# Kernel tuning notes

Hardware: AMD Instinct MI355X
Metric: run time of the kernel (lower is better)

## Reference

```python
import jax, jax.numpy as jnp
import numpy as np


def _conv2d_valid(x, w):
    # x: (N, C, H, W), w: (O, C, kH, kW) -> (N, O, H-kH+1, W-kW+1)
    return jax.lax.conv_general_dilated(
        x, w, window_strides=(1, 1), padding='VALID',
        dimension_numbers=('NCHW', 'OIHW', 'NCHW'))


def setup_inputs() -> dict:
    key = jax.random.key(0)
    kx, ky = jax.random.split(key)
    x = jax.random.normal(kx, (16, 64, 128, 128), dtype=jnp.float32)
    y = jax.random.normal(ky, (64, 64, 16, 16), dtype=jnp.float32)
    return {"x": x, "y": y}


def reference(x, y):
    # Normalize each of the K kernels to unit L2 norm (sum over C, kH, kW).
    normed_y = y / jnp.sqrt(jnp.sum(y * y, axis=(1, 2, 3), keepdims=True))
    # Per-window L2 norm of x via ones-kernel box conv over x^2.
    ones_kernel = jnp.ones(y.shape, dtype=x.dtype)
    x_norm = jnp.sqrt(_conv2d_valid(x * x, ones_kernel))
    # Normalized cross-correlation, clamped at zero.
    diss = _conv2d_valid(x, normed_y) / x_norm
    return jax.nn.relu(diss)
```

## Files before the change

kernel.cpp:

```cpp
#include <hip/hip_runtime.h>
#include <stdint.h>

#define GAS __attribute__((address_space(1)))
#define LAS __attribute__((address_space(3)))

typedef __attribute__((ext_vector_type(8))) short short8;
typedef __attribute__((ext_vector_type(4))) float float4v;
typedef __attribute__((ext_vector_type(4))) unsigned int uint4v;

__device__ __forceinline__ unsigned short f2bf(float f) {
  union { float f; unsigned int u; } v; v.f = f;
  unsigned int r = v.u + 0x7fffu + ((v.u >> 16) & 1u);
  return (unsigned short)(r >> 16);
}

__device__ __forceinline__ void async_g2l16(const void* g, void* l) {
  __builtin_amdgcn_global_load_lds((const GAS unsigned int*)g,
                                   (LAS unsigned int*)l, 16, 0, 0);
}

__device__ __forceinline__ void vmem_drain() {
  asm volatile("s_waitcnt vmcnt(0)" ::: "memory");
}

__global__ void knorm_y(const float* __restrict__ y, unsigned short* __restrict__ y_t2) {
  int o = blockIdx.x;
  int tid = threadIdx.x;
  const float* yo = y + o * 16384;
  float s = 0.f;
  for (int idx = tid; idx < 16384; idx += 256) { float v = yo[idx]; s += v * v; }
  for (int off = 32; off; off >>= 1) s += __shfl_down(s, off, 64);
  __shared__ float red[4];
  if ((tid & 63) == 0) red[tid >> 6] = s;
  __syncthreads();
  float rn = 1.0f / sqrtf(red[0] + red[1] + red[2] + red[3]);
  int og = o >> 4, ol = o & 15;
  for (int idx = tid; idx < 16384; idx += 256) {
    int c = idx >> 8, dy = (idx >> 4) & 15, dx = idx & 15;
    int t = dy * 16 + dx;
    int cb = c >> 5, q = (c >> 3) & 3, j = c & 7;
    size_t dst = (size_t)t * 4096 + (size_t)(og * 2 + cb) * 512 + (q * 16 + ol) * 8 + j;
    y_t2[dst] = f2bf(yo[idx] * rn);
  }
}

__global__ void ktrans_x(const float* __restrict__ x, unsigned short* __restrict__ x_t,
                         float* __restrict__ s) {
  int h = blockIdx.x, n = blockIdx.y;
  int tid = threadIdx.x;
  __shared__ __align__(16) unsigned short tb[8192];
  __shared__ float sb[256];
  const float* xb = x + ((size_t)n * 64) * 16384 + h * 128;
  int w = tid & 127, half = tid >> 7;
  float acc = 0.f;
#pragma unroll
  for (int cs = 0; cs < 4; ++cs) {
    short8 tmp;
#pragma unroll
    for (int j = 0; j < 8; ++j) {
      int c = half * 32 + cs * 8 + j;
      float v = xb[(size_t)c * 16384 + w];
      tmp[j] = (short)f2bf(v);
      acc += v * v;
    }
    int chunk = (half * 4 + cs) ^ (w & 7);
    *(short8*)(tb + w * 64 + chunk * 8) = tmp;
  }
  sb[tid] = acc;
  __syncthreads();
  uint4v* dst = (uint4v*)(x_t + ((size_t)(n * 128 + h)) * 8192);
  const uint4v* src = (const uint4v*)tb;
  for (int idx = tid; idx < 1024; idx += 256) dst[idx] = src[idx];
  if (tid < 128) s[((size_t)(n * 128 + h)) * 128 + tid] = sb[tid] + sb[tid + 128];
}

__global__ void knorm_x(const float* __restrict__ s, float* __restrict__ invn) {
  int i = blockIdx.x, n = blockIdx.y;
  int tid = threadIdx.x;
  __shared__ float colsum[128];
  const float* sp = s + ((size_t)(n * 128 + i)) * 128;
  float a = 0.f;
#pragma unroll
  for (int dy = 0; dy < 16; ++dy) a += sp[dy * 128 + tid];
  colsum[tid] = a;
  __syncthreads();
  if (tid < 113) {
    float acc = 0.f;
#pragma unroll
    for (int dx = 0; dx < 16; ++dx) acc += colsum[tid + dx];
    invn[((size_t)n * 113 + i) * 113 + tid] = 1.0f / sqrtf(acc);
  }
}

__launch_bounds__(256, 3)
__global__ void kconv(const unsigned short* __restrict__ x_t,
                      const unsigned short* __restrict__ y_t2,
                      const float* __restrict__ invn,
                      float* __restrict__ out) {
  int lin = blockIdx.y * 113 + blockIdx.x;
  int npair = lin & 7;
  int i = lin >> 3;
  int n0 = npair * 2;
  int tid = threadIdx.x;
  int lane = tid & 63, wave = tid >> 6;
  int lane15 = lane & 15, q = lane >> 4;
  int nn = wave >> 1;
  int jh = wave & 1;

  __shared__ __align__(16) char smem[34816];

  auto stageA2 = [&](int dy) {
#pragma unroll
    for (int r = 0; r < 2; ++r) {
      const char* src = (const char*)(x_t + ((size_t)((n0 + r) * 128 + i + dy)) * 8192);
#pragma unroll
      for (int it = 0; it < 4; ++it) {
        int chunk = it * 256 + wave * 64;
        async_g2l16(src + (chunk + lane) * 16, smem + r * 16384 + chunk * 16);
      }
    }
  };

  const short8* ybase = (const short8*)y_t2 + lane;
  auto loadB = [&](int t, short8 bf[4][2]) {
    const short8* p = ybase + (size_t)t * 512;
#pragma unroll
    for (int nt = 0; nt < 4; ++nt) {
      bf[nt][0] = p[nt * 128];
      bf[nt][1] = p[nt * 128 + 64];
    }
  };

  float4v acc[4][4];
#pragma unroll
  for (int mt = 0; mt < 4; ++mt)
#pragma unroll
    for (int nt = 0; nt < 4; ++nt) acc[mt][nt] = (float4v){0.f, 0.f, 0.f, 0.f};

  int abase[4];
#pragma unroll
  for (int mt = 0; mt < 4; ++mt)
    abase[mt] = nn * 16384 + (jh * 64 + mt * 16 + lane15) * 128;

  short8 b0[4][2], b1[4][2];
  stageA2(0);
  loadB(0, b0);
  vmem_drain();
  __syncthreads();

#pragma unroll 1
  for (int dy = 0; dy < 16; ++dy) {
#pragma unroll
    for (int dx = 0; dx < 16; ++dx) {
      int t = dy * 16 + dx;
      short8(&bc)[4][2] = (dx & 1) ? b1 : b0;
      short8(&bn)[4][2] = (dx & 1) ? b0 : b1;
      if (t < 255) loadB(t + 1, bn);
      int xr = (lane15 + dx) & 7;
#pragma unroll
      for (int cb = 0; cb < 2; ++cb) {
        int aoff = dx * 128 + (((q + cb * 4) ^ xr) << 4);
#pragma unroll
        for (int mt = 0; mt < 4; ++mt) {
          short8 a = *(const short8*)(smem + abase[mt] + aoff);
#pragma unroll
          for (int nt = 0; nt < 4; ++nt)
            acc[mt][nt] = __builtin_amdgcn_mfma_f32_16x16x32_bf16(a, bc[nt][cb], acc[mt][nt], 0, 0, 0);
        }
      }
    }
    if (dy < 15) {
      __syncthreads();
      stageA2(dy + 1);
      vmem_drain();
      __syncthreads();
    }
  }

  int n = n0 + nn;
  const float* ivp = invn + ((size_t)n * 113 + i) * 113;
  float* op = out + (size_t)n * 64 * 12769 + (size_t)i * 113;
  int jbase = jh * 64 + q * 4;
#pragma unroll
  for (int mt = 0; mt < 4; ++mt) {
    int j0 = jbase + mt * 16;
    if (j0 <= 108) {
      float4v iv = *(const float4v*)(ivp + j0);
#pragma unroll
      for (int nt = 0; nt < 4; ++nt) {
        int o = nt * 16 + lane15;
        float4v v = acc[mt][nt];
        float4v r;
        r[0] = fmaxf(v[0] * iv[0], 0.f);
        r[1] = fmaxf(v[1] * iv[1], 0.f);
        r[2] = fmaxf(v[2] * iv[2], 0.f);
        r[3] = fmaxf(v[3] * iv[3], 0.f);
        *(float4v*)(op + (size_t)o * 12769 + j0) = r;
      }
    } else if (j0 == 112) {
      float ivs = ivp[112];
#pragma unroll
      for (int nt = 0; nt < 4; ++nt) {
        int o = nt * 16 + lane15;
        op[(size_t)o * 12769 + 112] = fmaxf(acc[mt][nt][0] * ivs, 0.f);
      }
    }
  }
}

extern "C" void kernel_launch(void* const* d_in, const int* in_sizes, int n_in,
                              void* d_out, int out_size, void* d_ws, size_t ws_size,
                              hipStream_t stream) {
  const float* x = (const float*)d_in[0];
  const float* y = (const float*)d_in[1];
  float* out = (float*)d_out;
  char* ws = (char*)d_ws;
  unsigned short* x_t = (unsigned short*)ws;
  unsigned short* y_t2 = (unsigned short*)(ws + 33554432);
  float* s = (float*)(ws + 35651584);
  float* invn = (float*)(ws + 36700160);

  hipLaunchKernelGGL(knorm_y, dim3(64), dim3(256), 0, stream, y, y_t2);
  hipLaunchKernelGGL(ktrans_x, dim3(128, 16), dim3(256), 0, stream, x, x_t, s);
  hipLaunchKernelGGL(knorm_x, dim3(113, 16), dim3(128), 0, stream, s, invn);
  hipLaunchKernelGGL(kconv, dim3(113, 8), dim3(256), 0, stream, x_t, y_t2, invn, out);
}
```

Measured before the change: 600.4 us.

## Tile conv blocks over two output rows of one image with triple-buffered row prefetch

Measured after the change: 609.1 us. No clear change (+1.4%).

```diff
diff --git a/kernel.cpp b/kernel.cpp
--- a/kernel.cpp
+++ b/kernel.cpp
@@ -97,37 +97,38 @@
                       const unsigned short* __restrict__ y_t2,
                       const float* __restrict__ invn,
                       float* __restrict__ out) {
-  int lin = blockIdx.y * 113 + blockIdx.x;
-  int npair = lin & 7;
-  int i = lin >> 3;
-  int n0 = npair * 2;
+  int lin = blockIdx.y * 57 + blockIdx.x;
+  int wg = (lin & 7) * 114 + (lin >> 3);
+  int p = wg % 57;
+  int n = wg / 57;
+  int i0 = p * 2;
   int tid = threadIdx.x;
   int lane = tid & 63, wave = tid >> 6;
   int lane15 = lane & 15, q = lane >> 4;
-  int nn = wave >> 1;
+  int iw = wave >> 1;
   int jh = wave & 1;
 
-  __shared__ __align__(16) char smem[34816];
-
-  auto stageA2 = [&](int dy) {
-#pragma unroll
-    for (int r = 0; r < 2; ++r) {
-      const char* src = (const char*)(x_t + ((size_t)((n0 + r) * 128 + i + dy)) * 8192);
-#pragma unroll
-      for (int it = 0; it < 4; ++it) {
-        int chunk = it * 256 + wave * 64;
-        async_g2l16(src + (chunk + lane) * 16, smem + r * 16384 + chunk * 16);
-      }
+  __shared__ __align__(16) char smem[49152];
+
+  const char* xbase = (const char*)x_t + ((size_t)n * 128) * 16384;
+
+  auto stageRow = [&](int h, int k) {
+    const char* src = xbase + (size_t)h * 16384;
+    char* buf = smem + k * 16384;
+#pragma unroll
+    for (int it = 0; it < 4; ++it) {
+      int chunk = it * 256 + wave * 64;
+      async_g2l16(src + (chunk + lane) * 16, buf + chunk * 16);
     }
   };
 
   const short8* ybase = (const short8*)y_t2 + lane;
   auto loadB = [&](int t, short8 bf[4][2]) {
-    const short8* p = ybase + (size_t)t * 512;
+    const short8* pt = ybase + (size_t)t * 512;
 #pragma unroll
     for (int nt = 0; nt < 4; ++nt) {
-      bf[nt][0] = p[nt * 128];
-      bf[nt][1] = p[nt * 128 + 64];
+      bf[nt][0] = pt[nt * 128];
+      bf[nt][1] = pt[nt * 128 + 64];
     }
   };
 
@@ -140,16 +141,27 @@
   int abase[4];
 #pragma unroll
   for (int mt = 0; mt < 4; ++mt)
-    abase[mt] = nn * 16384 + (jh * 64 + mt * 16 + lane15) * 128;
+    abase[mt] = (jh * 64 + mt * 16 + lane15) * 128;
 
   short8 b0[4][2], b1[4][2];
-  stageA2(0);
+  stageRow(i0, 0);
+  stageRow(i0 + 1, 1);
   loadB(0, b0);
   vmem_drain();
   __syncthreads();
 
+  int r0 = 0;
 #pragma unroll 1
   for (int dy = 0; dy < 16; ++dy) {
+    if (dy < 15) {
+      int h = i0 + dy + 2;
+      if (h > 127) h = 127;
+      __builtin_amdgcn_sched_barrier(0);
+      stageRow(h, r0 + 2 >= 3 ? r0 - 1 : r0 + 2);
+      __builtin_amdgcn_sched_barrier(0);
+    }
+    int rb = r0 + iw >= 3 ? r0 + iw - 3 : r0 + iw;
+    const char* Ab = smem + rb * 16384;
 #pragma unroll
     for (int dx = 0; dx < 16; ++dx) {
       int t = dy * 16 + dx;
@@ -162,47 +174,46 @@
         int aoff = dx * 128 + (((q + cb * 4) ^ xr) << 4);
 #pragma unroll
         for (int mt = 0; mt < 4; ++mt) {
-          short8 a = *(const short8*)(smem + abase[mt] + aoff);
+          short8 a = *(const short8*)(Ab + abase[mt] + aoff);
 #pragma unroll
           for (int nt = 0; nt < 4; ++nt)
             acc[mt][nt] = __builtin_amdgcn_mfma_f32_16x16x32_bf16(a, bc[nt][cb], acc[mt][nt], 0, 0, 0);
         }
       }
     }
-    if (dy < 15) {
-      __syncthreads();
-      stageA2(dy + 1);
-      vmem_drain();
-      __syncthreads();
-    }
-  }
-
-  int n = n0 + nn;
-  const float* ivp = invn + ((size_t)n * 113 + i) * 113;
-  float* op = out + (size_t)n * 64 * 12769 + (size_t)i * 113;
-  int jbase = jh * 64 + q * 4;
-#pragma unroll
-  for (int mt = 0; mt < 4; ++mt) {
-    int j0 = jbase + mt * 16;
-    if (j0 <= 108) {
-      float4v iv = *(const float4v*)(ivp + j0);
-#pragma unroll
-      for (int nt = 0; nt < 4; ++nt) {
-        int o = nt * 16 + lane15;
-        float4v v = acc[mt][nt];
-        float4v r;
-        r[0] = fmaxf(v[0] * iv[0], 0.f);
-        r[1] = fmaxf(v[1] * iv[1], 0.f);
-        r[2] = fmaxf(v[2] * iv[2], 0.f);
-        r[3] = fmaxf(v[3] * iv[3], 0.f);
-        *(float4v*)(op + (size_t)o * 12769 + j0) = r;
-      }
-    } else if (j0 == 112) {
-      float ivs = ivp[112];
-#pragma unroll
-      for (int nt = 0; nt < 4; ++nt) {
-        int o = nt * 16 + lane15;
-        op[(size_t)o * 12769 + 112] = fmaxf(acc[mt][nt][0] * ivs, 0.f);
+    asm volatile("s_waitcnt vmcnt(8)" ::: "memory");
+    __syncthreads();
+    r0 = r0 == 2 ? 0 : r0 + 1;
+  }
+
+  int i = i0 + iw;
+  if (i <= 112) {
+    const float* ivp = invn + ((size_t)n * 113 + i) * 113;
+    float* op = out + (size_t)n * 64 * 12769 + (size_t)i * 113;
+    int jbase = jh * 64 + q * 4;
+#pragma unroll
+    for (int mt = 0; mt < 4; ++mt) {
+      int j0 = jbase + mt * 16;
+      if (j0 <= 108) {
+        float4v iv = *(const float4v*)(ivp + j0);
+#pragma unroll
+        for (int nt = 0; nt < 4; ++nt) {
+          int o = nt * 16 + lane15;
+          float4v v = acc[mt][nt];
+          float4v r;
+          r[0] = fmaxf(v[0] * iv[0], 0.f);
+          r[1] = fmaxf(v[1] * iv[1], 0.f);
+          r[2] = fmaxf(v[2] * iv[2], 0.f);
+          r[3] = fmaxf(v[3] * iv[3], 0.f);
+          *(float4v*)(op + (size_t)o * 12769 + j0) = r;
+        }
+      } else if (j0 == 112) {
+        float ivs = ivp[112];
+#pragma unroll
+        for (int nt = 0; nt < 4; ++nt) {
+          int o = nt * 16 + lane15;
+          op[(size_t)o * 12769 + 112] = fmaxf(acc[mt][nt][0] * ivs, 0.f);
+        }
       }
     }
   }
@@ -223,5 +234,5 @@
   hipLaunchKernelGGL(knorm_y, dim3(64), dim3(256), 0, stream, y, y_t2);
   hipLaunchKernelGGL(ktrans_x, dim3(128, 16), dim3(256), 0, stream, x, x_t, s);
   hipLaunchKernelGGL(knorm_x, dim3(113, 16), dim3(128), 0, stream, s, invn);
-  hipLaunchKernelGGL(kconv, dim3(113, 8), dim3(256), 0, stream, x_t, y_t2, invn, out);
-}
+  hipLaunchKernelGGL(kconv, dim3(57, 16), dim3(256), 0, stream, x_t, y_t2, invn, out);
+}
```
